# Optimization experiments

Measured on AMD Instinct MI355X. Metric: run time of the kernel, lower is better.

The kernel has to match this reference:

```python
import jax, jax.numpy as jnp
import numpy as np

B = 16384
IN = 128
H = 128
NC = 10
NATT = 3
EPS = 1e-5


def setup_inputs() -> dict:
    key = jax.random.key(0)
    ks = jax.random.split(key, 8)
    s_in = 1.0 / np.sqrt(IN)
    s_h = 1.0 / np.sqrt(H)
    return {
        "x": jax.random.normal(ks[0], (B, IN), dtype=jnp.float32),
        "W_in": jax.random.uniform(ks[1], (IN, H), jnp.float32, -s_in, s_in),
        "b_in": jax.random.uniform(ks[2], (H,), jnp.float32, -s_in, s_in),
        "W_att": jax.random.uniform(ks[3], (NATT, H, H), jnp.float32, -s_h, s_h),
        "b_att": jax.random.uniform(ks[4], (NATT, H), jnp.float32, -s_h, s_h),
        "gamma": jnp.ones((NATT, H), jnp.float32),
        "beta": jnp.zeros((NATT, H), jnp.float32),
        "W_c": jax.random.uniform(ks[5], (H, NC), jnp.float32, -s_h, s_h),
        "b_c": jax.random.uniform(ks[6], (NC,), jnp.float32, -s_h, s_h),
    }


def _layernorm(y, g, b):
    mu = jnp.mean(y, axis=-1, keepdims=True)
    var = jnp.mean((y - mu) ** 2, axis=-1, keepdims=True)
    return (y - mu) * jax.lax.rsqrt(var + EPS) * g + b


def reference(x, W_in, b_in, W_att, b_att, gamma, beta, W_c, b_c):
    # in_proj: [B, IN] -> [B, H]
    h = x @ W_in + b_in
    for i in range(NATT):
        u = jnp.tanh(h @ W_att[i] + b_att[i])            # [B, H]
        scores = u[:, :, None] * u[:, None, :]            # outer product [B, H, H]
        attn = jax.nn.softmax(scores, axis=-1)
        out = jnp.einsum("bij,bj->bi", attn, h)          # [B, H]
        h = _layernorm(h + out, gamma[i], beta[i])
    return h @ W_c + b_c                                  # [B, NC]
```

## Files before the change

kernel.cpp:

```cpp
#include <hip/hip_runtime.h>
#include <math.h>

#define B_TOT 16384
#define H     128
#define NC    10
#define NATT  3
#define TR    16
#define HBS   136
#define KT    5
#define EPS   1e-5f

typedef __attribute__((ext_vector_type(8))) short bf16x8;
typedef __attribute__((ext_vector_type(4))) float f32x4;

__device__ __forceinline__ ushort f2bf(float f) {
    union { float f; unsigned u; } v; v.f = f;
    unsigned r = v.u + 0x7fffu + ((v.u >> 16) & 1u);
    return (ushort)(r >> 16);
}

__device__ __forceinline__ float fast_tanh(float a) {
    a = fminf(15.f, fmaxf(-15.f, a));
    float t = __expf(2.f * a);
    return (t - 1.f) / (t + 1.f);
}

template<int CTRL>
__device__ __forceinline__ float dpp_add(float v) {
    int x = __float_as_int(v);
    int y = __builtin_amdgcn_update_dpp(0, x, CTRL, 0xf, 0xf, false);
    return v + __int_as_float(y);
}
__device__ __forceinline__ float red16(float v) {
    v = dpp_add<0x121>(v);
    v = dpp_add<0x122>(v);
    v = dpp_add<0x124>(v);
    v = dpp_add<0x128>(v);
    return v;
}

extern "C" __global__ __launch_bounds__(256)
void prep_weights(const float* __restrict__ W_in,
                  const float* __restrict__ W_att,
                  const float* __restrict__ W_c,
                  ushort* __restrict__ wt)
{
    int i = blockIdx.x * 256 + threadIdx.x;
    if (i < 65536) {
        int mat = i >> 14, idx = i & 16383;
        int k = idx >> 7, n = idx & 127;
        float v = (mat == 0) ? W_in[idx] : W_att[(mat - 1) * 16384 + idx];
        wt[mat * 16384 + n * H + k] = f2bf(v);
    } else if (i < 65536 + 2048) {
        int idx = i - 65536;
        int n = idx >> 7, k = idx & 127;
        float v = (n < NC) ? W_c[k * NC + n] : 0.f;
        wt[65536 + n * H + k] = f2bf(v);
    }
}

extern "C" __global__ __launch_bounds__(128, 2)
void simple_attention_kernel(const float* __restrict__ x,
                             const float* __restrict__ b_in,
                             const float* __restrict__ b_att,
                             const float* __restrict__ gamma,
                             const float* __restrict__ beta,
                             const float* __restrict__ b_c,
                             const ushort* __restrict__ wt,
                             float* __restrict__ out)
{
    __shared__ __align__(16) ushort ab[TR * HBS];
    __shared__ __align__(16) float  exm[2 * 16 * 12];
    __shared__ __align__(16) float  exl[2 * 16 * 2];

    const int tid  = threadIdx.x;
    const int wv   = tid >> 6;
    const int lane = tid & 63;
    const int s    = lane & 15;
    const int q    = lane >> 4;
    const size_t rowBase = (size_t)blockIdx.x * TR;

    float h[4][4];
    f32x4 acc[4];

    {
        bf16x8 af[4];
        #pragma unroll
        for (int ks = 0; ks < 4; ++ks) {
            const float* xp = x + (rowBase + s) * H + ks * 32 + q * 8;
            float4 v0 = *(const float4*)xp;
            float4 v1 = *(const float4*)(xp + 4);
            bf16x8 a;
            a[0] = f2bf(v0.x); a[1] = f2bf(v0.y); a[2] = f2bf(v0.z); a[3] = f2bf(v0.w);
            a[4] = f2bf(v1.x); a[5] = f2bf(v1.y); a[6] = f2bf(v1.z); a[7] = f2bf(v1.w);
            af[ks] = a;
        }
        #pragma unroll
        for (int t = 0; t < 4; ++t) acc[t] = (f32x4){0.f, 0.f, 0.f, 0.f};
        #pragma unroll
        for (int ks = 0; ks < 4; ++ks) {
            #pragma unroll
            for (int t = 0; t < 4; ++t) {
                bf16x8 b = *(const bf16x8*)&wt[(64 * wv + 16 * t + s) * H + ks * 32 + q * 8];
                acc[t] = __builtin_amdgcn_mfma_f32_16x16x32_bf16(af[ks], b, acc[t], 0, 0, 0);
            }
        }
        #pragma unroll
        for (int t = 0; t < 4; ++t) {
            int n = 64 * wv + 16 * t + s;
            float bi = b_in[n];
            #pragma unroll
            for (int r = 0; r < 4; ++r) {
                h[t][r] = acc[t][r] + bi;
                ab[(4 * q + r) * HBS + n] = f2bf(h[t][r]);
            }
        }
        __syncthreads();
    }

    const float cm[KT] = {1.00004478f, 0.99730768f, 0.49919676f, 0.17734736f, 0.04379392f};

    #pragma unroll 1
    for (int layer = 0; layer < NATT; ++layer) {
        const ushort* WT = wt + (size_t)(1 + layer) * 16384;

        bf16x8 af[4];
        #pragma unroll
        for (int ks = 0; ks < 4; ++ks)
            af[ks] = *(const bf16x8*)&ab[s * HBS + ks * 32 + q * 8];
        #pragma unroll
        for (int t = 0; t < 4; ++t) acc[t] = (f32x4){0.f, 0.f, 0.f, 0.f};
        #pragma unroll
        for (int ks = 0; ks < 4; ++ks) {
            #pragma unroll
            for (int t = 0; t < 4; ++t) {
                bf16x8 b = *(const bf16x8*)&WT[(64 * wv + 16 * t + s) * H + ks * 32 + q * 8];
                acc[t] = __builtin_amdgcn_mfma_f32_16x16x32_bf16(af[ks], b, acc[t], 0, 0, 0);
            }
        }
        float u[4][4];
        #pragma unroll
        for (int t = 0; t < 4; ++t) {
            float ba = b_att[layer * H + 64 * wv + 16 * t + s];
            #pragma unroll
            for (int r = 0; r < 4; ++r) u[t][r] = fast_tanh(acc[t][r] + ba);
        }

        float S[4][KT], T[4][KT - 1];
        #pragma unroll
        for (int r = 0; r < 4; ++r) {
            #pragma unroll
            for (int k = 0; k < KT; ++k) S[r][k] = 0.f;
            #pragma unroll
            for (int k = 0; k < KT - 1; ++k) T[r][k] = 0.f;
        }
        #pragma unroll
        for (int t = 0; t < 4; ++t) {
            #pragma unroll
            for (int r = 0; r < 4; ++r) {
                float uu = u[t][r], hh = h[t][r];
                S[r][0] += hh;
                float p = uu;
                S[r][1] += p * hh; T[r][0] += p;
                #pragma unroll
                for (int k = 2; k < KT; ++k) {
                    p *= uu;
                    S[r][k] += p * hh;
                    T[r][k - 1] += p;
                }
            }
        }
        #pragma unroll
        for (int r = 0; r < 4; ++r) {
            #pragma unroll
            for (int k = 0; k < KT; ++k)     S[r][k] = red16(S[r][k]);
            #pragma unroll
            for (int k = 0; k < KT - 1; ++k) T[r][k] = red16(T[r][k]);
        }
        if (s == 0) {
            #pragma unroll
            for (int r = 0; r < 4; ++r) {
                float* dst = &exm[(wv * 16 + 4 * q + r) * 12];
                *(f32x4*)&dst[0] = (f32x4){S[r][0], S[r][1], S[r][2], S[r][3]};
                *(f32x4*)&dst[4] = (f32x4){S[r][4], T[r][0], T[r][1], T[r][2]};
                dst[8] = T[r][3];
            }
        }
        __syncthreads();
        #pragma unroll
        for (int r = 0; r < 4; ++r) {
            const float* src = &exm[((1 - wv) * 16 + 4 * q + r) * 12];
            f32x4 c0 = *(const f32x4*)&src[0];
            f32x4 c1 = *(const f32x4*)&src[4];
            float c2 = src[8];
            S[r][0] = (S[r][0] + c0.x) * cm[0];
            S[r][1] = (S[r][1] + c0.y) * cm[1];
            S[r][2] = (S[r][2] + c0.z) * cm[2];
            S[r][3] = (S[r][3] + c0.w) * cm[3];
            S[r][4] = (S[r][4] + c1.x) * cm[4];
            T[r][0] = (T[r][0] + c1.y) * cm[1];
            T[r][1] = (T[r][1] + c1.z) * cm[2];
            T[r][2] = (T[r][2] + c1.w) * cm[3];
            T[r][3] = (T[r][3] + c2)   * cm[4];
        }

        float ls[4] = {0,0,0,0}, lq[4] = {0,0,0,0};
        #pragma unroll
        for (int t = 0; t < 4; ++t) {
            #pragma unroll
            for (int r = 0; r < 4; ++r) {
                float uu = u[t][r];
                float num = S[r][KT - 1];
                #pragma unroll
                for (int k = KT - 2; k >= 0; --k) num = num * uu + S[r][k];
                float den = T[r][KT - 2];
                #pragma unroll
                for (int k = KT - 3; k >= 0; --k) den = den * uu + T[r][k];
                den = den * uu + 128.f * 1.00004478f;
                float yy = h[t][r] + num * __builtin_amdgcn_rcpf(den);
                h[t][r] = yy;
                ls[r] += yy; lq[r] += yy * yy;
            }
        }
        #pragma unroll
        for (int r = 0; r < 4; ++r) { ls[r] = red16(ls[r]); lq[r] = red16(lq[r]); }
        if (s == 0) {
            #pragma unroll
            for (int r = 0; r < 4; ++r)
                *(float2*)&exl[(wv * 16 + 4 * q + r) * 2] = make_float2(ls[r], lq[r]);
        }
        __syncthreads();
        float mu[4], inv[4];
        #pragma unroll
        for (int r = 0; r < 4; ++r) {
            float2 o = *(const float2*)&exl[((1 - wv) * 16 + 4 * q + r) * 2];
            float sm = ls[r] + o.x, sq = lq[r] + o.y;
            mu[r] = sm * (1.f / H);
            float var = sq * (1.f / H) - mu[r] * mu[r];
            inv[r] = rsqrtf(var + EPS);
        }
        #pragma unroll
        for (int t = 0; t < 4; ++t) {
            int n = 64 * wv + 16 * t + s;
            float g  = gamma[layer * H + n];
            float be = beta [layer * H + n];
            #pragma unroll
            for (int r = 0; r < 4; ++r) {
                float hn = (h[t][r] - mu[r]) * inv[r] * g + be;
                h[t][r] = hn;
                ab[(4 * q + r) * HBS + n] = f2bf(hn);
            }
        }
        __syncthreads();
    }

    if (wv == 0) {
        const ushort* WC = wt + 4 * 16384;
        f32x4 facc = (f32x4){0.f, 0.f, 0.f, 0.f};
        #pragma unroll
        for (int ks = 0; ks < 4; ++ks) {
            bf16x8 a = *(const bf16x8*)&ab[s * HBS + ks * 32 + q * 8];
            bf16x8 b = *(const bf16x8*)&WC[s * H + ks * 32 + q * 8];
            facc = __builtin_amdgcn_mfma_f32_16x16x32_bf16(a, b, facc, 0, 0, 0);
        }
        if (s < NC) {
            float bc = b_c[s];
            #pragma unroll
            for (int r = 0; r < 4; ++r)
                out[(rowBase + 4 * q + r) * NC + s] = facc[r] + bc;
        }
    }
}

extern "C" void kernel_launch(void* const* d_in, const int* in_sizes, int n_in,
                              void* d_out, int out_size, void* d_ws, size_t ws_size,
                              hipStream_t stream) {
    const float* x     = (const float*)d_in[0];
    const float* W_in  = (const float*)d_in[1];
    const float* b_in  = (const float*)d_in[2];
    const float* W_att = (const float*)d_in[3];
    const float* b_att = (const float*)d_in[4];
    const float* gamma = (const float*)d_in[5];
    const float* beta  = (const float*)d_in[6];
    const float* W_c   = (const float*)d_in[7];
    const float* b_c   = (const float*)d_in[8];
    float* out  = (float*)d_out;
    ushort* wt  = (ushort*)d_ws;

    hipLaunchKernelGGL(prep_weights, dim3(264), dim3(256), 0, stream,
                       W_in, W_att, W_c, wt);
    hipLaunchKernelGGL(simple_attention_kernel, dim3(B_TOT / TR), dim3(128), 0, stream,
                       x, b_in, b_att, gamma, beta, b_c, wt, out);
}
```

Baseline: 103.3 us.

## Split each 16-row tile across four waves and simplify tanh

Each block now runs four waves instead of two, and each wave owns 32 of the 128 hidden columns rather than 64. This halves per-thread MFMA work and register state. The input x is staged cooperatively into shared memory, and the cross-wave reductions for the polynomial softmax moments and the layernorm statistics now sum four partials from LDS. fast_tanh drops its clamp and uses a single reciprocal; this relies on rcp handling exp overflow to infinity correctly. The aim is more parallelism per tile and lower register pressure, at the cost of an extra barrier and more LDS reduction traffic.

```diff
diff --git a/kernel.cpp b/kernel.cpp
--- a/kernel.cpp
+++ b/kernel.cpp
@@ -20,9 +20,8 @@
 }
 
 __device__ __forceinline__ float fast_tanh(float a) {
-    a = fminf(15.f, fmaxf(-15.f, a));
     float t = __expf(2.f * a);
-    return (t - 1.f) / (t + 1.f);
+    return 1.f - 2.f * __builtin_amdgcn_rcpf(t + 1.f);
 }
 
 template<int CTRL>
@@ -59,7 +58,7 @@
     }
 }
 
-extern "C" __global__ __launch_bounds__(128, 2)
+extern "C" __global__ __launch_bounds__(256, 4)
 void simple_attention_kernel(const float* __restrict__ x,
                              const float* __restrict__ b_in,
                              const float* __restrict__ b_att,
@@ -70,8 +69,8 @@
                              float* __restrict__ out)
 {
     __shared__ __align__(16) ushort ab[TR * HBS];
-    __shared__ __align__(16) float  exm[2 * 16 * 12];
-    __shared__ __align__(16) float  exl[2 * 16 * 2];
+    __shared__ __align__(16) float  exm[4 * 16 * 12];
+    __shared__ __align__(16) float  exl[4 * 16 * 2];
 
     const int tid  = threadIdx.x;
     const int wv   = tid >> 6;
@@ -80,34 +79,39 @@
     const int q    = lane >> 4;
     const size_t rowBase = (size_t)blockIdx.x * TR;
 
-    float h[4][4];
-    f32x4 acc[4];
+    float h[2][4];
+    f32x4 acc[2];
+
+    {
+        const float* xp = x + (rowBase + s) * H + 32 * wv + q * 8;
+        float4 v0 = *(const float4*)xp;
+        float4 v1 = *(const float4*)(xp + 4);
+        bf16x8 a;
+        a[0] = f2bf(v0.x); a[1] = f2bf(v0.y); a[2] = f2bf(v0.z); a[3] = f2bf(v0.w);
+        a[4] = f2bf(v1.x); a[5] = f2bf(v1.y); a[6] = f2bf(v1.z); a[7] = f2bf(v1.w);
+        *(bf16x8*)&ab[s * HBS + 32 * wv + q * 8] = a;
+    }
+    __syncthreads();
 
     {
         bf16x8 af[4];
         #pragma unroll
+        for (int ks = 0; ks < 4; ++ks)
+            af[ks] = *(const bf16x8*)&ab[s * HBS + ks * 32 + q * 8];
+        #pragma unroll
+        for (int t = 0; t < 2; ++t) acc[t] = (f32x4){0.f, 0.f, 0.f, 0.f};
+        #pragma unroll
         for (int ks = 0; ks < 4; ++ks) {
-            const float* xp = x + (rowBase + s) * H + ks * 32 + q * 8;
-            float4 v0 = *(const float4*)xp;
-            float4 v1 = *(const float4*)(xp + 4);
-            bf16x8 a;
-            a[0] = f2bf(v0.x); a[1] = f2bf(v0.y); a[2] = f2bf(v0.z); a[3] = f2bf(v0.w);
-            a[4] = f2bf(v1.x); a[5] = f2bf(v1.y); a[6] = f2bf(v1.z); a[7] = f2bf(v1.w);
-            af[ks] = a;
-        }
-        #pragma unroll
-        for (int t = 0; t < 4; ++t) acc[t] = (f32x4){0.f, 0.f, 0.f, 0.f};
-        #pragma unroll
-        for (int ks = 0; ks < 4; ++ks) {
-            #pragma unroll
-            for (int t = 0; t < 4; ++t) {
-                bf16x8 b = *(const bf16x8*)&wt[(64 * wv + 16 * t + s) * H + ks * 32 + q * 8];
+            #pragma unroll
+            for (int t = 0; t < 2; ++t) {
+                bf16x8 b = *(const bf16x8*)&wt[(32 * wv + 16 * t + s) * H + ks * 32 + q * 8];
                 acc[t] = __builtin_amdgcn_mfma_f32_16x16x32_bf16(af[ks], b, acc[t], 0, 0, 0);
             }
         }
-        #pragma unroll
-        for (int t = 0; t < 4; ++t) {
-            int n = 64 * wv + 16 * t + s;
+        __syncthreads();
+        #pragma unroll
+        for (int t = 0; t < 2; ++t) {
+            int n = 32 * wv + 16 * t + s;
             float bi = b_in[n];
             #pragma unroll
             for (int r = 0; r < 4; ++r) {
@@ -129,19 +133,19 @@
         for (int ks = 0; ks < 4; ++ks)
             af[ks] = *(const bf16x8*)&ab[s * HBS + ks * 32 + q * 8];
         #pragma unroll
-        for (int t = 0; t < 4; ++t) acc[t] = (f32x4){0.f, 0.f, 0.f, 0.f};
+        for (int t = 0; t < 2; ++t) acc[t] = (f32x4){0.f, 0.f, 0.f, 0.f};
         #pragma unroll
         for (int ks = 0; ks < 4; ++ks) {
             #pragma unroll
-            for (int t = 0; t < 4; ++t) {
-                bf16x8 b = *(const bf16x8*)&WT[(64 * wv + 16 * t + s) * H + ks * 32 + q * 8];
+            for (int t = 0; t < 2; ++t) {
+                bf16x8 b = *(const bf16x8*)&WT[(32 * wv + 16 * t + s) * H + ks * 32 + q * 8];
                 acc[t] = __builtin_amdgcn_mfma_f32_16x16x32_bf16(af[ks], b, acc[t], 0, 0, 0);
             }
         }
-        float u[4][4];
-        #pragma unroll
-        for (int t = 0; t < 4; ++t) {
-            float ba = b_att[layer * H + 64 * wv + 16 * t + s];
+        float u[2][4];
+        #pragma unroll
+        for (int t = 0; t < 2; ++t) {
+            float ba = b_att[layer * H + 32 * wv + 16 * t + s];
             #pragma unroll
             for (int r = 0; r < 4; ++r) u[t][r] = fast_tanh(acc[t][r] + ba);
         }
@@ -155,7 +159,7 @@
             for (int k = 0; k < KT - 1; ++k) T[r][k] = 0.f;
         }
         #pragma unroll
-        for (int t = 0; t < 4; ++t) {
+        for (int t = 0; t < 2; ++t) {
             #pragma unroll
             for (int r = 0; r < 4; ++r) {
                 float uu = u[t][r], hh = h[t][r];
@@ -189,24 +193,30 @@
         __syncthreads();
         #pragma unroll
         for (int r = 0; r < 4; ++r) {
-            const float* src = &exm[((1 - wv) * 16 + 4 * q + r) * 12];
-            f32x4 c0 = *(const f32x4*)&src[0];
-            f32x4 c1 = *(const f32x4*)&src[4];
-            float c2 = src[8];
-            S[r][0] = (S[r][0] + c0.x) * cm[0];
-            S[r][1] = (S[r][1] + c0.y) * cm[1];
-            S[r][2] = (S[r][2] + c0.z) * cm[2];
-            S[r][3] = (S[r][3] + c0.w) * cm[3];
-            S[r][4] = (S[r][4] + c1.x) * cm[4];
-            T[r][0] = (T[r][0] + c1.y) * cm[1];
-            T[r][1] = (T[r][1] + c1.z) * cm[2];
-            T[r][2] = (T[r][2] + c1.w) * cm[3];
-            T[r][3] = (T[r][3] + c2)   * cm[4];
-        }
-
-        float ls[4] = {0,0,0,0}, lq[4] = {0,0,0,0};
-        #pragma unroll
-        for (int t = 0; t < 4; ++t) {
+            f32x4 s0 = (f32x4){0.f, 0.f, 0.f, 0.f};
+            f32x4 s1 = (f32x4){0.f, 0.f, 0.f, 0.f};
+            float s2 = 0.f;
+            #pragma unroll
+            for (int ow = 0; ow < 4; ++ow) {
+                const float* src = &exm[(ow * 16 + 4 * q + r) * 12];
+                s0 += *(const f32x4*)&src[0];
+                s1 += *(const f32x4*)&src[4];
+                s2 += src[8];
+            }
+            S[r][0] = s0.x * cm[0];
+            S[r][1] = s0.y * cm[1];
+            S[r][2] = s0.z * cm[2];
+            S[r][3] = s0.w * cm[3];
+            S[r][4] = s1.x * cm[4];
+            T[r][0] = s1.y * cm[1];
+            T[r][1] = s1.z * cm[2];
+            T[r][2] = s1.w * cm[3];
+            T[r][3] = s2   * cm[4];
+        }
+
+        float ls[4] = {0, 0, 0, 0}, lq[4] = {0, 0, 0, 0};
+        #pragma unroll
+        for (int t = 0; t < 2; ++t) {
             #pragma unroll
             for (int r = 0; r < 4; ++r) {
                 float uu = u[t][r];
@@ -233,15 +243,19 @@
         float mu[4], inv[4];
         #pragma unroll
         for (int r = 0; r < 4; ++r) {
-            float2 o = *(const float2*)&exl[((1 - wv) * 16 + 4 * q + r) * 2];
-            float sm = ls[r] + o.x, sq = lq[r] + o.y;
+            float sm = 0.f, sq = 0.f;
+            #pragma unroll
+            for (int ow = 0; ow < 4; ++ow) {
+                float2 o = *(const float2*)&exl[(ow * 16 + 4 * q + r) * 2];
+                sm += o.x; sq += o.y;
+            }
             mu[r] = sm * (1.f / H);
             float var = sq * (1.f / H) - mu[r] * mu[r];
             inv[r] = rsqrtf(var + EPS);
         }
         #pragma unroll
-        for (int t = 0; t < 4; ++t) {
-            int n = 64 * wv + 16 * t + s;
+        for (int t = 0; t < 2; ++t) {
+            int n = 32 * wv + 16 * t + s;
             float g  = gamma[layer * H + n];
             float be = beta [layer * H + n];
             #pragma unroll
@@ -289,6 +303,6 @@
 
     hipLaunchKernelGGL(prep_weights, dim3(264), dim3(256), 0, stream,
                        W_in, W_att, W_c, wt);
-    hipLaunchKernelGGL(simple_attention_kernel, dim3(B_TOT / TR), dim3(128), 0, stream,
+    hipLaunchKernelGGL(simple_attention_kernel, dim3(B_TOT / TR), dim3(256), 0, stream,
                        x, b_in, b_att, gamma, beta, b_c, wt, out);
 }
```

Result: no change. 104.6 us (+1.2%).

## Split each 16-row tile across eight waves with LDS cross-wave reductions

Applied to the files above, without the earlier changes.

Each block now runs 512 threads (eight waves), and each wave owns a single 16-column slice of the hidden dimension instead of two waves each owning 64 columns. The polynomial-softmax moment sums and the layernorm statistics are combined across the eight waves through padded LDS buffers, using a DPP reduction over the eight partials. The input tile is staged into LDS by four waves before the first projection. tanh is also simplified to one reciprocal with no clamping. The intent is more parallelism and fewer registers per thread to raise occupancy, at the cost of extra barriers, more LDS traffic and an extra reduction stage.

```diff
diff --git a/kernel.cpp b/kernel.cpp
--- a/kernel.cpp
+++ b/kernel.cpp
@@ -9,6 +9,8 @@
 #define HBS   136
 #define KT    5
 #define EPS   1e-5f
+#define EXM_CS 196
+#define EXL_CS 34
 
 typedef __attribute__((ext_vector_type(8))) short bf16x8;
 typedef __attribute__((ext_vector_type(4))) float f32x4;
@@ -20,9 +22,8 @@
 }
 
 __device__ __forceinline__ float fast_tanh(float a) {
-    a = fminf(15.f, fmaxf(-15.f, a));
     float t = __expf(2.f * a);
-    return (t - 1.f) / (t + 1.f);
+    return 1.f - 2.f * __builtin_amdgcn_rcpf(t + 1.f);
 }
 
 template<int CTRL>
@@ -36,6 +37,12 @@
     v = dpp_add<0x122>(v);
     v = dpp_add<0x124>(v);
     v = dpp_add<0x128>(v);
+    return v;
+}
+__device__ __forceinline__ float red8ror(float v) {
+    v = dpp_add<0x121>(v);
+    v = dpp_add<0x122>(v);
+    v = dpp_add<0x124>(v);
     return v;
 }
 
@@ -59,7 +66,7 @@
     }
 }
 
-extern "C" __global__ __launch_bounds__(128, 2)
+extern "C" __global__ __launch_bounds__(512, 8)
 void simple_attention_kernel(const float* __restrict__ x,
                              const float* __restrict__ b_in,
                              const float* __restrict__ b_att,
@@ -70,8 +77,8 @@
                              float* __restrict__ out)
 {
     __shared__ __align__(16) ushort ab[TR * HBS];
-    __shared__ __align__(16) float  exm[2 * 16 * 12];
-    __shared__ __align__(16) float  exl[2 * 16 * 2];
+    __shared__ __align__(16) float  exm[8 * EXM_CS];
+    __shared__ __align__(16) float  exl[8 * EXL_CS];
 
     const int tid  = threadIdx.x;
     const int wv   = tid >> 6;
@@ -79,41 +86,39 @@
     const int s    = lane & 15;
     const int q    = lane >> 4;
     const size_t rowBase = (size_t)blockIdx.x * TR;
-
-    float h[4][4];
-    f32x4 acc[4];
+    const int colN = 16 * wv + s;
+
+    float h[4];
+    f32x4 acc;
+
+    if (wv < 4) {
+        const float* xp = x + (rowBase + s) * H + 32 * wv + q * 8;
+        float4 v0 = *(const float4*)xp;
+        float4 v1 = *(const float4*)(xp + 4);
+        bf16x8 a;
+        a[0] = f2bf(v0.x); a[1] = f2bf(v0.y); a[2] = f2bf(v0.z); a[3] = f2bf(v0.w);
+        a[4] = f2bf(v1.x); a[5] = f2bf(v1.y); a[6] = f2bf(v1.z); a[7] = f2bf(v1.w);
+        *(bf16x8*)&ab[s * HBS + 32 * wv + q * 8] = a;
+    }
+    __syncthreads();
 
     {
         bf16x8 af[4];
         #pragma unroll
+        for (int ks = 0; ks < 4; ++ks)
+            af[ks] = *(const bf16x8*)&ab[s * HBS + ks * 32 + q * 8];
+        acc = (f32x4){0.f, 0.f, 0.f, 0.f};
+        #pragma unroll
         for (int ks = 0; ks < 4; ++ks) {
-            const float* xp = x + (rowBase + s) * H + ks * 32 + q * 8;
-            float4 v0 = *(const float4*)xp;
-            float4 v1 = *(const float4*)(xp + 4);
-            bf16x8 a;
-            a[0] = f2bf(v0.x); a[1] = f2bf(v0.y); a[2] = f2bf(v0.z); a[3] = f2bf(v0.w);
-            a[4] = f2bf(v1.x); a[5] = f2bf(v1.y); a[6] = f2bf(v1.z); a[7] = f2bf(v1.w);
-            af[ks] = a;
-        }
-        #pragma unroll
-        for (int t = 0; t < 4; ++t) acc[t] = (f32x4){0.f, 0.f, 0.f, 0.f};
-        #pragma unroll
-        for (int ks = 0; ks < 4; ++ks) {
-            #pragma unroll
-            for (int t = 0; t < 4; ++t) {
-                bf16x8 b = *(const bf16x8*)&wt[(64 * wv + 16 * t + s) * H + ks * 32 + q * 8];
-                acc[t] = __builtin_amdgcn_mfma_f32_16x16x32_bf16(af[ks], b, acc[t], 0, 0, 0);
-            }
-        }
-        #pragma unroll
-        for (int t = 0; t < 4; ++t) {
-            int n = 64 * wv + 16 * t + s;
-            float bi = b_in[n];
-            #pragma unroll
-            for (int r = 0; r < 4; ++r) {
-                h[t][r] = acc[t][r] + bi;
-                ab[(4 * q + r) * HBS + n] = f2bf(h[t][r]);
-            }
+            bf16x8 b = *(const bf16x8*)&wt[colN * H + ks * 32 + q * 8];
+            acc = __builtin_amdgcn_mfma_f32_16x16x32_bf16(af[ks], b, acc, 0, 0, 0);
+        }
+        __syncthreads();
+        float bi = b_in[colN];
+        #pragma unroll
+        for (int r = 0; r < 4; ++r) {
+            h[r] = acc[r] + bi;
+            ab[(4 * q + r) * HBS + colN] = f2bf(h[r]);
         }
         __syncthreads();
     }
@@ -128,59 +133,42 @@
         #pragma unroll
         for (int ks = 0; ks < 4; ++ks)
             af[ks] = *(const bf16x8*)&ab[s * HBS + ks * 32 + q * 8];
-        #pragma unroll
-        for (int t = 0; t < 4; ++t) acc[t] = (f32x4){0.f, 0.f, 0.f, 0.f};
+        acc = (f32x4){0.f, 0.f, 0.f, 0.f};
         #pragma unroll
         for (int ks = 0; ks < 4; ++ks) {
-            #pragma unroll
-            for (int t = 0; t < 4; ++t) {
-                bf16x8 b = *(const bf16x8*)&WT[(64 * wv + 16 * t + s) * H + ks * 32 + q * 8];
-                acc[t] = __builtin_amdgcn_mfma_f32_16x16x32_bf16(af[ks], b, acc[t], 0, 0, 0);
+            bf16x8 b = *(const bf16x8*)&WT[colN * H + ks * 32 + q * 8];
+            acc = __builtin_amdgcn_mfma_f32_16x16x32_bf16(af[ks], b, acc, 0, 0, 0);
+        }
+        float ba = b_att[layer * H + colN];
+        float u[4];
+        #pragma unroll
+        for (int r = 0; r < 4; ++r) u[r] = fast_tanh(acc[r] + ba);
+
+        float S[4][KT], T[4][KT - 1];
+        #pragma unroll
+        for (int r = 0; r < 4; ++r) {
+            float uu = u[r], hh = h[r];
+            S[r][0] = hh;
+            float p = uu;
+            S[r][1] = p * hh; T[r][0] = p;
+            #pragma unroll
+            for (int k = 2; k < KT; ++k) {
+                p *= uu;
+                S[r][k] = p * hh;
+                T[r][k - 1] = p;
             }
         }
-        float u[4][4];
-        #pragma unroll
-        for (int t = 0; t < 4; ++t) {
-            float ba = b_att[layer * H + 64 * wv + 16 * t + s];
-            #pragma unroll
-            for (int r = 0; r < 4; ++r) u[t][r] = fast_tanh(acc[t][r] + ba);
-        }
-
-        float S[4][KT], T[4][KT - 1];
-        #pragma unroll
-        for (int r = 0; r < 4; ++r) {
-            #pragma unroll
-            for (int k = 0; k < KT; ++k) S[r][k] = 0.f;
-            #pragma unroll
-            for (int k = 0; k < KT - 1; ++k) T[r][k] = 0.f;
-        }
-        #pragma unroll
-        for (int t = 0; t < 4; ++t) {
+        #pragma unroll
+        for (int r = 0; r < 4; ++r) {
+            #pragma unroll
+            for (int k = 0; k < KT; ++k)     S[r][k] = red16(S[r][k]);
+            #pragma unroll
+            for (int k = 0; k < KT - 1; ++k) T[r][k] = red16(T[r][k]);
+        }
+        if (s == 0) {
             #pragma unroll
             for (int r = 0; r < 4; ++r) {
-                float uu = u[t][r], hh = h[t][r];
-                S[r][0] += hh;
-                float p = uu;
-                S[r][1] += p * hh; T[r][0] += p;
-                #pragma unroll
-                for (int k = 2; k < KT; ++k) {
-                    p *= uu;
-                    S[r][k] += p * hh;
-                    T[r][k - 1] += p;
-                }
-            }
-        }
-        #pragma unroll
-        for (int r = 0; r < 4; ++r) {
-            #pragma unroll
-            for (int k = 0; k < KT; ++k)     S[r][k] = red16(S[r][k]);
-            #pragma unroll
-            for (int k = 0; k < KT - 1; ++k) T[r][k] = red16(T[r][k]);
-        }
-        if (s == 0) {
-            #pragma unroll
-            for (int r = 0; r < 4; ++r) {
-                float* dst = &exm[(wv * 16 + 4 * q + r) * 12];
+                float* dst = &exm[wv * EXM_CS + (4 * q + r) * 12];
                 *(f32x4*)&dst[0] = (f32x4){S[r][0], S[r][1], S[r][2], S[r][3]};
                 *(f32x4*)&dst[4] = (f32x4){S[r][4], T[r][0], T[r][1], T[r][2]};
                 dst[8] = T[r][3];
@@ -189,67 +177,58 @@
         __syncthreads();
         #pragma unroll
         for (int r = 0; r < 4; ++r) {
-            const float* src = &exm[((1 - wv) * 16 + 4 * q + r) * 12];
+            const float* src = &exm[(s & 7) * EXM_CS + (4 * q + r) * 12];
             f32x4 c0 = *(const f32x4*)&src[0];
             f32x4 c1 = *(const f32x4*)&src[4];
             float c2 = src[8];
-            S[r][0] = (S[r][0] + c0.x) * cm[0];
-            S[r][1] = (S[r][1] + c0.y) * cm[1];
-            S[r][2] = (S[r][2] + c0.z) * cm[2];
-            S[r][3] = (S[r][3] + c0.w) * cm[3];
-            S[r][4] = (S[r][4] + c1.x) * cm[4];
-            T[r][0] = (T[r][0] + c1.y) * cm[1];
-            T[r][1] = (T[r][1] + c1.z) * cm[2];
-            T[r][2] = (T[r][2] + c1.w) * cm[3];
-            T[r][3] = (T[r][3] + c2)   * cm[4];
-        }
-
-        float ls[4] = {0,0,0,0}, lq[4] = {0,0,0,0};
-        #pragma unroll
-        for (int t = 0; t < 4; ++t) {
-            #pragma unroll
-            for (int r = 0; r < 4; ++r) {
-                float uu = u[t][r];
-                float num = S[r][KT - 1];
-                #pragma unroll
-                for (int k = KT - 2; k >= 0; --k) num = num * uu + S[r][k];
-                float den = T[r][KT - 2];
-                #pragma unroll
-                for (int k = KT - 3; k >= 0; --k) den = den * uu + T[r][k];
-                den = den * uu + 128.f * 1.00004478f;
-                float yy = h[t][r] + num * __builtin_amdgcn_rcpf(den);
-                h[t][r] = yy;
-                ls[r] += yy; lq[r] += yy * yy;
-            }
-        }
-        #pragma unroll
-        for (int r = 0; r < 4; ++r) { ls[r] = red16(ls[r]); lq[r] = red16(lq[r]); }
+            S[r][0] = red8ror(c0.x) * cm[0];
+            S[r][1] = red8ror(c0.y) * cm[1];
+            S[r][2] = red8ror(c0.z) * cm[2];
+            S[r][3] = red8ror(c0.w) * cm[3];
+            S[r][4] = red8ror(c1.x) * cm[4];
+            T[r][0] = red8ror(c1.y) * cm[1];
+            T[r][1] = red8ror(c1.z) * cm[2];
+            T[r][2] = red8ror(c1.w) * cm[3];
+            T[r][3] = red8ror(c2)   * cm[4];
+        }
+
+        #pragma unroll
+        for (int r = 0; r < 4; ++r) {
+            float uu = u[r];
+            float num = S[r][KT - 1];
+            #pragma unroll
+            for (int k = KT - 2; k >= 0; --k) num = num * uu + S[r][k];
+            float den = T[r][KT - 2];
+            #pragma unroll
+            for (int k = KT - 3; k >= 0; --k) den = den * uu + T[r][k];
+            den = den * uu + 128.f * 1.00004478f;
+            h[r] = h[r] + num * __builtin_amdgcn_rcpf(den);
+        }
+
+        float lsv[4], lqv[4];
+        #pragma unroll
+        for (int r = 0; r < 4; ++r) {
+            lsv[r] = red16(h[r]);
+            lqv[r] = red16(h[r] * h[r]);
+        }
         if (s == 0) {
             #pragma unroll
             for (int r = 0; r < 4; ++r)
-                *(float2*)&exl[(wv * 16 + 4 * q + r) * 2] = make_float2(ls[r], lq[r]);
-        }
-        __syncthreads();
-        float mu[4], inv[4];
-        #pragma unroll
-        for (int r = 0; r < 4; ++r) {
-            float2 o = *(const float2*)&exl[((1 - wv) * 16 + 4 * q + r) * 2];
-            float sm = ls[r] + o.x, sq = lq[r] + o.y;
-            mu[r] = sm * (1.f / H);
-            float var = sq * (1.f / H) - mu[r] * mu[r];
-            inv[r] = rsqrtf(var + EPS);
-        }
-        #pragma unroll
-        for (int t = 0; t < 4; ++t) {
-            int n = 64 * wv + 16 * t + s;
-            float g  = gamma[layer * H + n];
-            float be = beta [layer * H + n];
-            #pragma unroll
-            for (int r = 0; r < 4; ++r) {
-                float hn = (h[t][r] - mu[r]) * inv[r] * g + be;
-                h[t][r] = hn;
-                ab[(4 * q + r) * HBS + n] = f2bf(hn);
-            }
+                *(float2*)&exl[wv * EXL_CS + (4 * q + r) * 2] = make_float2(lsv[r], lqv[r]);
+        }
+        __syncthreads();
+        float g  = gamma[layer * H + colN];
+        float be = beta [layer * H + colN];
+        #pragma unroll
+        for (int r = 0; r < 4; ++r) {
+            float2 o = *(const float2*)&exl[(s & 7) * EXL_CS + (4 * q + r) * 2];
+            float sm = red8ror(o.x), sq = red8ror(o.y);
+            float mu = sm * (1.f / H);
+            float var = sq * (1.f / H) - mu * mu;
+            float inv = rsqrtf(var + EPS);
+            float hn = (h[r] - mu) * inv * g + be;
+            h[r] = hn;
+            ab[(4 * q + r) * HBS + colN] = f2bf(hn);
         }
         __syncthreads();
     }
@@ -289,6 +268,6 @@
 
     hipLaunchKernelGGL(prep_weights, dim3(264), dim3(256), 0, stream,
                        W_in, W_att, W_c, wt);
-    hipLaunchKernelGGL(simple_attention_kernel, dim3(B_TOT / TR), dim3(128), 0, stream,
+    hipLaunchKernelGGL(simple_attention_kernel, dim3(B_TOT / TR), dim3(512), 0, stream,
                        x, b_in, b_att, gamma, beta, b_c, wt, out);
 }
```

After: 166.0 us. +60.7%, slower.
